# Performance work log

Measured on AMD Instinct MI355X. Metric: run time of the kernel, lower is better.

Reference implementation:

```python
import jax, jax.numpy as jnp
import numpy as np

G, B, DEG, BATCH = 4000, 8, 32, 128  # genes, per-gene layersize, off-diag blocks/gene, batch


def setup_inputs() -> dict:
    key = jax.random.key(0)
    rng = np.random.default_rng(0)
    # block structure: DEG off-diagonal PPI blocks per gene + reflexive diagonal
    src = np.repeat(np.arange(G, dtype=np.int32), DEG)
    off = 1 + rng.integers(0, G - 1, size=G * DEG)          # never 0 -> off-diagonal
    dst = ((src.astype(np.int64) + off) % G).astype(np.int32)
    diag = np.arange(G, dtype=np.int32)
    block_in = jnp.asarray(np.concatenate([src, diag]))      # [N] = [G*DEG + G]
    block_out = jnp.asarray(np.concatenate([dst, diag]))     # [N]
    n_blocks = G * DEG + G
    k1, k2 = jax.random.split(key)
    x = jax.random.normal(k1, (BATCH, G * B), dtype=jnp.float32)
    w = jax.random.normal(k2, (n_blocks, B, B), dtype=jnp.float32) * 0.05
    return {"x": x, "w": w, "block_in": block_in, "block_out": block_out}


def reference(x, w, block_in, block_out):
    batch, d = x.shape
    n_blocks, b, _ = w.shape
    g = d // b
    xb = x.reshape(batch, g, b)
    xin = xb[:, block_in, :]                        # [batch, N, b] irregular gather
    contrib = jnp.einsum('bni,nio->nbo', xin, w)    # [N, batch, b] tiny per-block GEMMs
    out = jax.ops.segment_sum(contrib, block_out, num_segments=g)  # [g, batch, b] scatter-add
    out = jnp.transpose(out, (1, 0, 2)).reshape(batch, d)
    # activation_function is identity (default lambda x: x); residual=True
    return out + x
```

## Files before the change

kernel.cpp:

```cpp
#include <hip/hip_runtime.h>
#include <hip/hip_bf16.h>

#define G      4000
#define DEG    32
#define BATCH  128
#define D      32000
#define NBLK   132000
#define ZBLK   NBLK
#define CAP    96
#define SCAP   112

typedef __attribute__((ext_vector_type(8))) short bf16x8;
typedef __attribute__((ext_vector_type(4))) float f32x4;

__device__ inline unsigned bf16rne(float f) {
    unsigned u = __float_as_uint(f);
    return (u + 0x7fffu + ((u >> 16) & 1u)) >> 16;
}

#define NB_BUILD 516
#define NB_TR    1000
#define NB_W     2063

__global__ __launch_bounds__(256) void prep_kernel(const float* __restrict__ x,
                                                   const float* __restrict__ w,
                                                   const int* __restrict__ block_in,
                                                   const int* __restrict__ block_out,
                                                   int* __restrict__ cnt,
                                                   int2* __restrict__ pairs,
                                                   unsigned short* __restrict__ xgb,
                                                   unsigned short* __restrict__ wtb) {
    __shared__ float shmem[64 * 68];
    const int bid = blockIdx.x;
    const int t   = threadIdx.x;

    if (bid < NB_BUILD) {
        int n = bid * 256 + t;
        if (n < NBLK) {
            int dst = block_out[n];
            int src = block_in[n];
            int pos = atomicAdd(&cnt[dst], 1);
            if (pos < CAP) pairs[dst * CAP + pos] = make_int2(n, src);
        }
    } else if (bid < NB_BUILD + NB_TR) {
        int id = bid - NB_BUILD;
        int c0 = (id % 250) * 128;
        int b0 = (id / 250) * 32;
        int half = (b0 >= 64) ? 1 : 0;
        int lr0  = b0 & 63;
#pragma unroll
        for (int it = 0; it < 4; ++it) {
            int l  = it * 1024 + t * 4;
            int br = l >> 7;
            int c  = l & 127;
            float4 v = *(const float4*)(x + (size_t)(b0 + br) * D + c0 + c);
            *(float4*)&shmem[br * 132 + c] = v;
        }
        __syncthreads();
#pragma unroll
        for (int it = 0; it < 2; ++it) {
            int idx = it * 256 + t;
            int gl  = idx >> 5;
            int bl  = idx & 31;
            float4 v0 = *(const float4*)&shmem[bl * 132 + gl * 8];
            float4 v1 = *(const float4*)&shmem[bl * 132 + gl * 8 + 4];
            uint4 p;
            p.x = bf16rne(v0.x) | (bf16rne(v0.y) << 16);
            p.y = bf16rne(v0.z) | (bf16rne(v0.w) << 16);
            p.z = bf16rne(v1.x) | (bf16rne(v1.y) << 16);
            p.w = bf16rne(v1.z) | (bf16rne(v1.w) << 16);
            int gidx = (c0 >> 3) + gl;
            size_t base = (((size_t)half * G + gidx) * 64 + lr0 + bl) * 8;
            *(uint4*)(xgb + base) = p;
        }
    } else {
        int    id       = bid - (NB_BUILD + NB_TR);
        size_t base_blk = (size_t)id * 64;
        const float* wb = w + base_blk * 64;
#pragma unroll
        for (int j = 0; j < 4; ++j) {
            int pos  = j * 1024 + t * 4;
            int nl   = pos >> 6;
            int rest = pos & 63;
            float4 v;
            if (base_blk + nl < NBLK) v = *(const float4*)(wb + pos);
            else                      v = make_float4(0.f, 0.f, 0.f, 0.f);
            *(float4*)&shmem[nl * 68 + rest] = v;
        }
        __syncthreads();
#pragma unroll
        for (int j = 0; j < 2; ++j) {
            int p  = j * 256 + t;
            int nl = p >> 3;
            int o  = p & 7;
            size_t nglob = base_blk + nl;
            if (nglob <= NBLK) {
                const float* r = &shmem[nl * 68 + o];
                uint4 q;
                q.x = bf16rne(r[0])  | (bf16rne(r[8])  << 16);
                q.y = bf16rne(r[16]) | (bf16rne(r[24]) << 16);
                q.z = bf16rne(r[32]) | (bf16rne(r[40]) << 16);
                q.w = bf16rne(r[48]) | (bf16rne(r[56]) << 16);
                *(uint4*)(wtb + nglob * 64 + o * 8) = q;
            }
        }
    }
}

__global__ __launch_bounds__(128) void compute_kernel(const float* __restrict__ x,
                                                      const unsigned short* __restrict__ xgb,
                                                      const unsigned short* __restrict__ wtb,
                                                      const int2* __restrict__ pairs,
                                                      const int* __restrict__ cnt,
                                                      float* __restrict__ out) {
    const int blk  = blockIdx.x;
    const int half = (blk & 7) >> 2;
    const int g    = (blk >> 3) * 4 + (blk & 3);
    const int t    = threadIdx.x;
    const int wave = t >> 6;
    const int lane = t & 63;
    const int quad = lane >> 4;
    const int lo16 = lane & 15;

    __shared__ int2  se[SCAP];
    __shared__ uint4 wl[SCAP * 8];

    int m = cnt[g];
    if (m > CAP) m = CAP;

    if (t < SCAP) {
        int2 e = (t < m) ? pairs[(size_t)g * CAP + t] : make_int2(ZBLK, 0);
        se[t] = e;
    }

    int epad = (m + 15) & ~15;
    if (epad > SCAP) epad = SCAP;
    for (int e0 = 0; e0 < epad; e0 += 16) {
        int idx = e0 * 8 + t;
        int e   = e0 + (t >> 3);
        int j   = t & 7;
        int n   = (e < m) ? pairs[(size_t)g * CAP + e].x : ZBLK;
        wl[idx] = *(const uint4*)(wtb + ((size_t)n << 6) + j * 8);
    }
    __syncthreads();

    const int ob    = lo16 & 7;
    const int mt0   = wave * 32 + lo16;
    const int a0off = mt0 * 8;
    const int a1off = a0off + 128;
    const size_t hbase = (size_t)half * G;

    f32x4 acc0 = {0.f, 0.f, 0.f, 0.f};
    f32x4 acc1 = {0.f, 0.f, 0.f, 0.f};

#define LOADA(k0, A0, A1)                                                 \
    do {                                                                  \
        int s_ = se[(k0) + quad].y;                                       \
        const unsigned short* xb_ = xgb + ((hbase + s_) << 9);            \
        A0 = *(const uint4*)(xb_ + a0off);                                \
        A1 = *(const uint4*)(xb_ + a1off);                                \
    } while (0)

#define CONS(k0, A0, A1)                                                  \
    do {                                                                  \
        uint4 BB = wl[((k0) + quad) * 8 + ob];                            \
        acc0 = __builtin_amdgcn_mfma_f32_16x16x32_bf16(                   \
            __builtin_bit_cast(bf16x8, A0), __builtin_bit_cast(bf16x8, BB), acc0, 0, 0, 0); \
        acc1 = __builtin_amdgcn_mfma_f32_16x16x32_bf16(                   \
            __builtin_bit_cast(bf16x8, A1), __builtin_bit_cast(bf16x8, BB), acc1, 0, 0, 0); \
    } while (0)

    uint4 Pa0, Pa1, Qa0, Qa1, Ra0, Ra1, Sa0, Sa1;

    LOADA(0,  Pa0, Pa1);
    LOADA(4,  Qa0, Qa1);
    LOADA(8,  Ra0, Ra1);
    LOADA(12, Sa0, Sa1);

    for (int k0 = 0; k0 < m; k0 += 16) {
        CONS(k0, Pa0, Pa1);
        LOADA(k0 + 16, Pa0, Pa1);
        CONS(k0 + 4, Qa0, Qa1);
        LOADA(k0 + 20, Qa0, Qa1);
        CONS(k0 + 8, Ra0, Ra1);
        LOADA(k0 + 24, Ra0, Ra1);
        CONS(k0 + 12, Sa0, Sa1);
        LOADA(k0 + 28, Sa0, Sa1);
    }

    if (lo16 < 8) {
        const int col = g * 8 + lo16;
#pragma unroll
        for (int r = 0; r < 4; ++r) {
            int row0 = half * 64 + wave * 32 + quad * 4 + r;
            int row1 = row0 + 16;
            out[(size_t)row0 * D + col] = acc0[r] + x[(size_t)row0 * D + col];
            out[(size_t)row1 * D + col] = acc1[r] + x[(size_t)row1 * D + col];
        }
    }
#undef LOADA
#undef CONS
}

extern "C" void kernel_launch(void* const* d_in, const int* in_sizes, int n_in,
                              void* d_out, int out_size, void* d_ws, size_t ws_size,
                              hipStream_t stream) {
    const float* x         = (const float*)d_in[0];
    const float* w         = (const float*)d_in[1];
    const int*   block_in  = (const int*)d_in[2];
    const int*   block_out = (const int*)d_in[3];
    float*       out       = (float*)d_out;

    char* ws = (char*)d_ws;
    int*            cnt   = (int*)ws;
    int2*           pairs = (int2*)(ws + 16384);
    unsigned short* xgb   = (unsigned short*)(ws + 3088384);
    unsigned short* wtb   = (unsigned short*)(ws + 11280384);

    hipMemsetAsync(cnt, 0, 16384, stream);
    prep_kernel<<<NB_BUILD + NB_TR + NB_W, 256, 0, stream>>>(x, w, block_in, block_out,
                                                             cnt, pairs, xgb, wtb);
    compute_kernel<<<G * 2, 128, 0, stream>>>(x, xgb, wtb, pairs, cnt, out);
}
```

Baseline: 143.3 us.

## Fuse weight bf16 conversion into compute kernel, drop prep weight pass

The separate prep pass that converted and transposed all weights to bf16 in workspace is removed. The compute kernel now gathers each block's fp32 weights directly, converts them to bf16 with a strided transpose, and writes them to shared memory. This removes one full read and write of the bf16 weight buffer. In exchange, each weight is read twice (once per batch-half block) with strided, less coalesced fp32 loads, and an extra barrier is added.

```diff
diff --git a/kernel.cpp b/kernel.cpp
--- a/kernel.cpp
+++ b/kernel.cpp
@@ -6,7 +6,6 @@
 #define BATCH  128
 #define D      32000
 #define NBLK   132000
-#define ZBLK   NBLK
 #define CAP    96
 #define SCAP   112
 
@@ -20,17 +19,14 @@
 
 #define NB_BUILD 516
 #define NB_TR    1000
-#define NB_W     2063
 
 __global__ __launch_bounds__(256) void prep_kernel(const float* __restrict__ x,
-                                                   const float* __restrict__ w,
                                                    const int* __restrict__ block_in,
                                                    const int* __restrict__ block_out,
                                                    int* __restrict__ cnt,
                                                    int2* __restrict__ pairs,
-                                                   unsigned short* __restrict__ xgb,
-                                                   unsigned short* __restrict__ wtb) {
-    __shared__ float shmem[64 * 68];
+                                                   unsigned short* __restrict__ xgb) {
+    __shared__ float shmem[32 * 132];
     const int bid = blockIdx.x;
     const int t   = threadIdx.x;
 
@@ -42,7 +38,7 @@
             int pos = atomicAdd(&cnt[dst], 1);
             if (pos < CAP) pairs[dst * CAP + pos] = make_int2(n, src);
         }
-    } else if (bid < NB_BUILD + NB_TR) {
+    } else {
         int id = bid - NB_BUILD;
         int c0 = (id % 250) * 128;
         int b0 = (id / 250) * 32;
@@ -73,43 +69,12 @@
             size_t base = (((size_t)half * G + gidx) * 64 + lr0 + bl) * 8;
             *(uint4*)(xgb + base) = p;
         }
-    } else {
-        int    id       = bid - (NB_BUILD + NB_TR);
-        size_t base_blk = (size_t)id * 64;
-        const float* wb = w + base_blk * 64;
-#pragma unroll
-        for (int j = 0; j < 4; ++j) {
-            int pos  = j * 1024 + t * 4;
-            int nl   = pos >> 6;
-            int rest = pos & 63;
-            float4 v;
-            if (base_blk + nl < NBLK) v = *(const float4*)(wb + pos);
-            else                      v = make_float4(0.f, 0.f, 0.f, 0.f);
-            *(float4*)&shmem[nl * 68 + rest] = v;
-        }
-        __syncthreads();
-#pragma unroll
-        for (int j = 0; j < 2; ++j) {
-            int p  = j * 256 + t;
-            int nl = p >> 3;
-            int o  = p & 7;
-            size_t nglob = base_blk + nl;
-            if (nglob <= NBLK) {
-                const float* r = &shmem[nl * 68 + o];
-                uint4 q;
-                q.x = bf16rne(r[0])  | (bf16rne(r[8])  << 16);
-                q.y = bf16rne(r[16]) | (bf16rne(r[24]) << 16);
-                q.z = bf16rne(r[32]) | (bf16rne(r[40]) << 16);
-                q.w = bf16rne(r[48]) | (bf16rne(r[56]) << 16);
-                *(uint4*)(wtb + nglob * 64 + o * 8) = q;
-            }
-        }
     }
 }
 
 __global__ __launch_bounds__(128) void compute_kernel(const float* __restrict__ x,
                                                       const unsigned short* __restrict__ xgb,
-                                                      const unsigned short* __restrict__ wtb,
+                                                      const float* __restrict__ w,
                                                       const int2* __restrict__ pairs,
                                                       const int* __restrict__ cnt,
                                                       float* __restrict__ out) {
@@ -129,18 +94,28 @@
     if (m > CAP) m = CAP;
 
     if (t < SCAP) {
-        int2 e = (t < m) ? pairs[(size_t)g * CAP + t] : make_int2(ZBLK, 0);
+        int2 e = (t < m) ? pairs[(size_t)g * CAP + t] : make_int2(0, 0);
         se[t] = e;
     }
+    __syncthreads();
 
-    int epad = (m + 15) & ~15;
-    if (epad > SCAP) epad = SCAP;
-    for (int e0 = 0; e0 < epad; e0 += 16) {
-        int idx = e0 * 8 + t;
-        int e   = e0 + (t >> 3);
-        int j   = t & 7;
-        int n   = (e < m) ? pairs[(size_t)g * CAP + e].x : ZBLK;
-        wl[idx] = *(const uint4*)(wtb + ((size_t)n << 6) + j * 8);
+#pragma unroll
+    for (int r = 0; r < 7; ++r) {
+        int idx = r * 128 + t;
+        int e   = idx >> 3;
+        int o   = idx & 7;
+        uint4 q = {0u, 0u, 0u, 0u};
+        if (e < m) {
+            int n = se[e].x;
+            const float* wp = w + ((size_t)n << 6) + o;
+            float v0 = wp[0],  v1 = wp[8],  v2 = wp[16], v3 = wp[24];
+            float v4 = wp[32], v5 = wp[40], v6 = wp[48], v7 = wp[56];
+            q.x = bf16rne(v0) | (bf16rne(v1) << 16);
+            q.y = bf16rne(v2) | (bf16rne(v3) << 16);
+            q.z = bf16rne(v4) | (bf16rne(v5) << 16);
+            q.w = bf16rne(v6) | (bf16rne(v7) << 16);
+        }
+        wl[idx] = q;
     }
     __syncthreads();
 
@@ -215,10 +190,9 @@
     int*            cnt   = (int*)ws;
     int2*           pairs = (int2*)(ws + 16384);
     unsigned short* xgb   = (unsigned short*)(ws + 3088384);
-    unsigned short* wtb   = (unsigned short*)(ws + 11280384);
 
     hipMemsetAsync(cnt, 0, 16384, stream);
-    prep_kernel<<<NB_BUILD + NB_TR + NB_W, 256, 0, stream>>>(x, w, block_in, block_out,
-                                                             cnt, pairs, xgb, wtb);
-    compute_kernel<<<G * 2, 128, 0, stream>>>(x, xgb, wtb, pairs, cnt, out);
+    prep_kernel<<<NB_BUILD + NB_TR, 256, 0, stream>>>(x, block_in, block_out,
+                                                      cnt, pairs, xgb);
+    compute_kernel<<<G * 2, 128, 0, stream>>>(x, xgb, w, pairs, cnt, out);
 }
```

New measurement: 143.5 us. About the same (+0.2%).
